# Kernel tuning notes

Measured on AMD Instinct MI355X. Metric: run time of the kernel, lower is better.

Reference implementation:

```python
import jax, jax.numpy as jnp
import numpy as np

N_POINTS = 1024
BETA = 0.75
N_IMP = int(BETA * N_POINTS)  # 768


def point_sample(feat, points):
    """Bilinear sample feat [B,C,H,W] at points [B,N,2] in [0,1] (x,y order).
    Matches F.grid_sample(feat, 2*points-1, align_corners=False, padding_mode='zeros')."""
    B, C, H, W = feat.shape
    gx = 2.0 * points[..., 0] - 1.0
    gy = 2.0 * points[..., 1] - 1.0
    # align_corners=False unnormalization
    x = ((gx + 1.0) * W - 1.0) * 0.5
    y = ((gy + 1.0) * H - 1.0) * 0.5
    x0 = jnp.floor(x)
    y0 = jnp.floor(y)
    wx = x - x0  # weight for x0+1
    wy = y - y0

    def gather(ix, iy):
        valid = (ix >= 0) & (ix <= W - 1) & (iy >= 0) & (iy <= H - 1)
        ixc = jnp.clip(ix, 0, W - 1).astype(jnp.int32)
        iyc = jnp.clip(iy, 0, H - 1).astype(jnp.int32)
        v = jax.vmap(lambda f, yy, xx: f[:, yy, xx])(feat, iyc, ixc)  # [B,C,N]
        return v * valid[:, None, :].astype(feat.dtype)

    v00 = gather(x0, y0)
    v01 = gather(x0 + 1, y0)
    v10 = gather(x0, y0 + 1)
    v11 = gather(x0 + 1, y0 + 1)
    wx_ = wx[:, None, :]
    wy_ = wy[:, None, :]
    return (v00 * (1 - wx_) * (1 - wy_) + v01 * wx_ * (1 - wy_)
            + v10 * (1 - wx_) * wy_ + v11 * wx_ * wy_)  # [B,C,N]


def sampling_points_train(coarse, over_gen, coverage):
    # sort channels descending per pixel, then sample the sorted map (PointRend)
    coarse_sorted = -jnp.sort(-coarse, axis=1)
    samp = point_sample(coarse_sorted, over_gen)  # [B,C,kN]
    uncertainty = -(samp[:, 0, :] - samp[:, 1, :])  # [B,kN]
    _, idx = jax.lax.top_k(uncertainty, N_IMP)  # [B,768]
    importance = jnp.take_along_axis(over_gen, idx[..., None], axis=1)  # [B,768,2]
    return jnp.concatenate([importance, coverage], axis=1)  # [B,1024,2]


def setup_inputs() -> dict:
    key = jax.random.key(0)
    ks = jax.random.split(key, 8)
    B = 16
    fine = jax.random.normal(ks[0], (B, 128, 256, 256), dtype=jnp.float32)
    coarse = jax.random.normal(ks[1], (B, 7, 64, 64), dtype=jnp.float32)
    w1 = jax.random.normal(ks[2], (135, 256), dtype=jnp.float32) * 0.05
    b1 = jnp.zeros((256,), dtype=jnp.float32)
    w2 = jax.random.normal(ks[3], (256, 7), dtype=jnp.float32) * 0.05
    b2 = jnp.zeros((7,), dtype=jnp.float32)
    over_gen = jax.random.uniform(ks[4], (B, 7 * N_POINTS, 2), dtype=jnp.float32)
    coverage = jax.random.uniform(ks[5], (B, N_POINTS - N_IMP, 2), dtype=jnp.float32)
    return {"fine": fine, "coarse": coarse, "w1": w1, "b1": b1,
            "w2": w2, "b2": b2, "over_gen": over_gen, "coverage": coverage}


def reference(fine, coarse, w1, b1, w2, b2, over_gen, coverage):
    points = sampling_points_train(coarse, over_gen, coverage)  # [B,1024,2]
    c = point_sample(coarse, points)  # [B,7,1024]
    f = point_sample(fine, points)    # [B,128,1024]
    feat = jnp.concatenate([c, f], axis=1).transpose(0, 2, 1)  # [B,1024,135]
    h = jax.nn.relu(jnp.einsum('bnc,cd->bnd', feat, w1) + b1)
    rend = (jnp.einsum('bnd,dk->bnk', h, w2) + b2).transpose(0, 2, 1)  # [B,7,1024]
    return rend, points
```

## Files before the change

kernel.cpp:

```cpp
#include <hip/hip_runtime.h>
#include <cstdint>
#include <cstddef>

#define PTS_OFF 114688

__global__ __launch_bounds__(1024) void select_points_kernel(
    const float* __restrict__ coarse,
    const float* __restrict__ over_gen,
    const float* __restrict__ coverage,
    float* out)
{
  const int b   = blockIdx.x;
  const int tid = threadIdx.x;

  __shared__ float sT1[4096];
  __shared__ float sT2[4096];
  __shared__ unsigned long long cand[1024];
  __shared__ unsigned int hist[1024];
  __shared__ int sSel;
  __shared__ int sRnew;
  __shared__ unsigned int sCnt;

  const float* cb = coarse + (size_t)b * 28672;
  for (int pix = tid; pix < 4096; pix += 1024) {
    float m1 = -INFINITY, m2 = -INFINITY;
#pragma unroll
    for (int ch = 0; ch < 7; ++ch) {
      float v = cb[ch * 4096 + pix];
      if (v > m1) { m2 = m1; m1 = v; }
      else if (v > m2) { m2 = v; }
    }
    sT1[pix] = m1;
    sT2[pix] = m2;
  }
  if (tid == 0) sCnt = 0u;
  __syncthreads();

  unsigned long long key[7];
  const float* og = over_gen + (size_t)b * 14336;
#pragma unroll
  for (int s = 0; s < 7; ++s) {
    int i = tid + s * 1024;
    float px = og[i * 2];
    float py = og[i * 2 + 1];
    float gx = __fsub_rn(__fmul_rn(2.0f, px), 1.0f);
    float gy = __fsub_rn(__fmul_rn(2.0f, py), 1.0f);
    float x  = __fmul_rn(__fsub_rn(__fmul_rn(__fadd_rn(gx, 1.0f), 64.0f), 1.0f), 0.5f);
    float y  = __fmul_rn(__fsub_rn(__fmul_rn(__fadd_rn(gy, 1.0f), 64.0f), 1.0f), 0.5f);
    float x0 = floorf(x), y0 = floorf(y);
    float wx = __fsub_rn(x, x0), wy = __fsub_rn(y, y0);
    float omwx = __fsub_rn(1.0f, wx), omwy = __fsub_rn(1.0f, wy);
    float x1 = x0 + 1.0f, y1 = y0 + 1.0f;

    float cxs[4] = {x0, x1, x0, x1};
    float cys[4] = {y0, y0, y1, y1};
    float t1[4], t2[4];
#pragma unroll
    for (int c = 0; c < 4; ++c) {
      bool valid = (cxs[c] >= 0.0f) && (cxs[c] <= 63.0f) &&
                   (cys[c] >= 0.0f) && (cys[c] <= 63.0f);
      int xi = (int)fminf(fmaxf(cxs[c], 0.0f), 63.0f);
      int yi = (int)fminf(fmaxf(cys[c], 0.0f), 63.0f);
      float m = valid ? 1.0f : 0.0f;
      int p = yi * 64 + xi;
      t1[c] = __fmul_rn(sT1[p], m);
      t2[c] = __fmul_rn(sT2[p], m);
    }
    float s0 = __fadd_rn(__fadd_rn(__fadd_rn(
        __fmul_rn(__fmul_rn(t1[0], omwx), omwy),
        __fmul_rn(__fmul_rn(t1[1], wx),   omwy)),
        __fmul_rn(__fmul_rn(t1[2], omwx), wy)),
        __fmul_rn(__fmul_rn(t1[3], wx),   wy));
    float s1 = __fadd_rn(__fadd_rn(__fadd_rn(
        __fmul_rn(__fmul_rn(t2[0], omwx), omwy),
        __fmul_rn(__fmul_rn(t2[1], wx),   omwy)),
        __fmul_rn(__fmul_rn(t2[2], omwx), wy)),
        __fmul_rn(__fmul_rn(t2[3], wx),   wy));
    float u = -__fsub_rn(s0, s1);
    unsigned int bits = __float_as_uint(u);
    unsigned int asc  = (bits & 0x80000000u) ? ~bits : (bits | 0x80000000u);
    unsigned int desc = ~asc;
    key[s] = ((unsigned long long)desc << 13) | (unsigned int)i;
  }

  unsigned int P = 0u;
  unsigned int r = 768u;
  const int sub = ((tid >> 6) & 3) << 8;
  for (int pos = 3; pos >= 0; --pos) {
    const int shift = pos * 8;
    hist[tid] = 0u;
    __syncthreads();
#pragma unroll
    for (int s = 0; s < 7; ++s) {
      unsigned int d = (unsigned int)(key[s] >> 13);
      if ((((d ^ P) >> shift) >> 8) == 0u) {
        atomicAdd(&hist[sub | ((d >> shift) & 255u)], 1u);
      }
    }
    __syncthreads();
    if (tid < 64) {
      unsigned int v0 = hist[tid*4]   + hist[256+tid*4]   + hist[512+tid*4]   + hist[768+tid*4];
      unsigned int v1 = hist[tid*4+1] + hist[256+tid*4+1] + hist[512+tid*4+1] + hist[768+tid*4+1];
      unsigned int v2 = hist[tid*4+2] + hist[256+tid*4+2] + hist[512+tid*4+2] + hist[768+tid*4+2];
      unsigned int v3 = hist[tid*4+3] + hist[256+tid*4+3] + hist[512+tid*4+3] + hist[768+tid*4+3];
      v1 += v0; v2 += v1; v3 += v2;
      unsigned int lanesum = v3;
      unsigned int inc = lanesum;
#pragma unroll
      for (int d = 1; d < 64; d <<= 1) {
        unsigned int tsum = __shfl_up(inc, d, 64);
        if (tid >= d) inc += tsum;
      }
      unsigned int excl = inc - lanesum;
      v0 += excl; v1 += excl; v2 += excl; v3 += excl;
      if (excl < r && r <= v0) { sSel = tid * 4;     sRnew = (int)(r - excl); }
      if (v0   < r && r <= v1) { sSel = tid * 4 + 1; sRnew = (int)(r - v0);   }
      if (v1   < r && r <= v2) { sSel = tid * 4 + 2; sRnew = (int)(r - v1);   }
      if (v2   < r && r <= v3) { sSel = tid * 4 + 3; sRnew = (int)(r - v2);   }
    }
    __syncthreads();
    P |= ((unsigned int)sSel) << shift;
    r = (unsigned int)sRnew;
  }

  cand[tid] = 0xFFFFFFFFFFFFFFFFull;
  __syncthreads();
#pragma unroll
  for (int s = 0; s < 7; ++s) {
    if ((unsigned int)(key[s] >> 13) <= P) {
      unsigned int p = atomicAdd(&sCnt, 1u);
      if (p < 1024u) cand[p] = key[s];
    }
  }
  __syncthreads();

  {
    unsigned long long e = cand[tid];
#pragma unroll
    for (int kk = 2; kk <= 64; kk <<= 1) {
      for (int j = kk >> 1; j >= 1; j >>= 1) {
        unsigned long long p = __shfl_xor(e, j, 64);
        bool up    = ((tid & kk) == 0);
        bool lower = ((tid & j) == 0);
        bool takemin = (lower == up);
        unsigned long long mn = (e < p) ? e : p;
        unsigned long long mx = (e < p) ? p : e;
        e = takemin ? mn : mx;
      }
    }
    cand[tid] = e;
    __syncthreads();

    for (int kk = 128; kk <= 1024; kk <<= 1) {
      for (int j = kk >> 1; j >= 64; j >>= 1) {
        int ixj = tid ^ j;
        if (ixj > tid) {
          unsigned long long a = cand[tid];
          unsigned long long c = cand[ixj];
          bool up = ((tid & kk) == 0);
          if ((a > c) == up) { cand[tid] = c; cand[ixj] = a; }
        }
        __syncthreads();
      }
      e = cand[tid];
      bool up = ((tid & kk) == 0);
#pragma unroll
      for (int j = 32; j >= 1; j >>= 1) {
        unsigned long long p = __shfl_xor(e, j, 64);
        bool lower = ((tid & j) == 0);
        bool takemin = (lower == up);
        unsigned long long mn = (e < p) ? e : p;
        unsigned long long mx = (e < p) ? p : e;
        e = takemin ? mn : mx;
      }
      cand[tid] = e;
      __syncthreads();
    }
  }

  float* po = out + PTS_OFF + (size_t)b * 2048;
  if (tid < 768) {
    unsigned int idx = (unsigned int)(cand[tid] & 0x1FFFu);
    po[tid * 2]     = og[idx * 2];
    po[tid * 2 + 1] = og[idx * 2 + 1];
  } else {
    int j = tid - 768;
    po[tid * 2]     = coverage[(size_t)b * 512 + j * 2];
    po[tid * 2 + 1] = coverage[(size_t)b * 512 + j * 2 + 1];
  }
}

__global__ __launch_bounds__(256) void point_head_kernel(
    const float* __restrict__ fine,
    const float* __restrict__ coarse,
    const float* __restrict__ gw1,
    const float* __restrict__ gb1,
    const float* __restrict__ gw2,
    const float* __restrict__ gb2,
    float* out)
{
  const int t   = threadIdx.x;
  const int blk = blockIdx.x;
  const int b   = blk >> 6;
  const int n0  = (blk & 63) * 16;

  __shared__ float sFeat[16][137];

  const float* pts = out + PTS_OFF + (size_t)b * 2048;
  const float* fb  = fine   + (size_t)b * 8388608;
  const float* cbs = coarse + (size_t)b * 28672;

  {
    const int pt = t & 15;
    const int cg = t >> 4;
    float px = pts[(n0 + pt) * 2];
    float py = pts[(n0 + pt) * 2 + 1];

    float gx = 2.0f * px - 1.0f;
    float gy = 2.0f * py - 1.0f;
    float x  = ((gx + 1.0f) * 256.0f - 1.0f) * 0.5f;
    float y  = ((gy + 1.0f) * 256.0f - 1.0f) * 0.5f;
    float x0f = floorf(x), y0f = floorf(y);
    float wx = x - x0f, wy = y - y0f;
    int ix0 = (int)x0f, iy0 = (int)y0f;
    int ix1 = ix0 + 1,  iy1 = iy0 + 1;
    float mx0 = (ix0 >= 0 && ix0 <= 255) ? 1.0f : 0.0f;
    float mx1 = (ix1 >= 0 && ix1 <= 255) ? 1.0f : 0.0f;
    float my0 = (iy0 >= 0 && iy0 <= 255) ? 1.0f : 0.0f;
    float my1 = (iy1 >= 0 && iy1 <= 255) ? 1.0f : 0.0f;
    int cx0 = min(max(ix0, 0), 255), cx1 = min(max(ix1, 0), 255);
    int cy0 = min(max(iy0, 0), 255), cy1 = min(max(iy1, 0), 255);
    float W00 = (1.0f - wx) * (1.0f - wy) * mx0 * my0;
    float W01 = wx * (1.0f - wy) * mx1 * my0;
    float W10 = (1.0f - wx) * wy * mx0 * my1;
    float W11 = wx * wy * mx1 * my1;
    int o00 = cy0 * 256 + cx0, o01 = cy0 * 256 + cx1;
    int o10 = cy1 * 256 + cx0, o11 = cy1 * 256 + cx1;

#pragma unroll
    for (int i = 0; i < 8; ++i) {
      int ch = cg * 8 + i;
      const float* f = fb + (size_t)ch * 65536;
      sFeat[pt][7 + ch] = f[o00] * W00 + f[o01] * W01 + f[o10] * W10 + f[o11] * W11;
    }

    if (cg == 0) {
      float cx  = ((gx + 1.0f) * 64.0f - 1.0f) * 0.5f;
      float cy  = ((gy + 1.0f) * 64.0f - 1.0f) * 0.5f;
      float cx0f = floorf(cx), cy0f = floorf(cy);
      float cwx = cx - cx0f, cwy = cy - cy0f;
      int jx0 = (int)cx0f, jy0 = (int)cy0f;
      int jx1 = jx0 + 1,   jy1 = jy0 + 1;
      float nx0 = (jx0 >= 0 && jx0 <= 63) ? 1.0f : 0.0f;
      float nx1 = (jx1 >= 0 && jx1 <= 63) ? 1.0f : 0.0f;
      float ny0 = (jy0 >= 0 && jy0 <= 63) ? 1.0f : 0.0f;
      float ny1 = (jy1 >= 0 && jy1 <= 63) ? 1.0f : 0.0f;
      int kx0 = min(max(jx0, 0), 63), kx1 = min(max(jx1, 0), 63);
      int ky0 = min(max(jy0, 0), 63), ky1 = min(max(jy1, 0), 63);
      float V00 = (1.0f - cwx) * (1.0f - cwy) * nx0 * ny0;
      float V01 = cwx * (1.0f - cwy) * nx1 * ny0;
      float V10 = (1.0f - cwx) * cwy * nx0 * ny1;
      float V11 = cwx * cwy * nx1 * ny1;
      int q00 = ky0 * 64 + kx0, q01 = ky0 * 64 + kx1;
      int q10 = ky1 * 64 + kx0, q11 = ky1 * 64 + kx1;
#pragma unroll
      for (int ch = 0; ch < 7; ++ch) {
        const float* c0 = cbs + ch * 4096;
        sFeat[pt][ch] = c0[q00] * V00 + c0[q01] * V01 + c0[q10] * V10 + c0[q11] * V11;
      }
    }
  }
  __syncthreads();

  const int lane = t & 63;
  const int wid  = t >> 6;
  const int p0   = wid * 4;

  float acc[4][4];
  {
    float bb0 = gb1[lane], bb1 = gb1[lane + 64];
    float bb2 = gb1[lane + 128], bb3 = gb1[lane + 192];
#pragma unroll
    for (int p = 0; p < 4; ++p) {
      acc[p][0] = bb0; acc[p][1] = bb1; acc[p][2] = bb2; acc[p][3] = bb3;
    }
  }
  for (int c = 0; c < 135; ++c) {
    const float* wr = gw1 + c * 256;
    float wv0 = wr[lane], wv1 = wr[lane + 64];
    float wv2 = wr[lane + 128], wv3 = wr[lane + 192];
#pragma unroll
    for (int p = 0; p < 4; ++p) {
      float fv = sFeat[p0 + p][c];
      acc[p][0] = fmaf(fv, wv0, acc[p][0]);
      acc[p][1] = fmaf(fv, wv1, acc[p][1]);
      acc[p][2] = fmaf(fv, wv2, acc[p][2]);
      acc[p][3] = fmaf(fv, wv3, acc[p][3]);
    }
  }

  float w2v[4][7];
#pragma unroll
  for (int rr = 0; rr < 4; ++rr) {
    const float* wr = gw2 + (size_t)(lane + 64 * rr) * 7;
#pragma unroll
    for (int k = 0; k < 7; ++k) w2v[rr][k] = wr[k];
  }
  float b2s = (lane < 7) ? gb2[lane] : 0.0f;

#pragma unroll
  for (int p = 0; p < 4; ++p) {
    float part[7];
#pragma unroll
    for (int k = 0; k < 7; ++k) part[k] = 0.0f;
#pragma unroll
    for (int rr = 0; rr < 4; ++rr) {
      float h = fmaxf(acc[p][rr], 0.0f);
#pragma unroll
      for (int k = 0; k < 7; ++k) part[k] = fmaf(h, w2v[rr][k], part[k]);
    }
#pragma unroll
    for (int k = 0; k < 7; ++k) {
      float s = part[k];
#pragma unroll
      for (int off = 32; off > 0; off >>= 1) s += __shfl_xor(s, off, 64);
      if (lane == k) out[((size_t)b * 7 + k) * 1024 + (n0 + p0 + p)] = s + b2s;
    }
  }
}

extern "C" void kernel_launch(void* const* d_in, const int* in_sizes, int n_in,
                              void* d_out, int out_size, void* d_ws, size_t ws_size,
                              hipStream_t stream) {
  (void)in_sizes; (void)n_in; (void)d_ws; (void)ws_size; (void)out_size;
  const float* fine     = (const float*)d_in[0];
  const float* coarse   = (const float*)d_in[1];
  const float* w1       = (const float*)d_in[2];
  const float* b1       = (const float*)d_in[3];
  const float* w2       = (const float*)d_in[4];
  const float* b2       = (const float*)d_in[5];
  const float* over_gen = (const float*)d_in[6];
  const float* coverage = (const float*)d_in[7];
  float* out = (float*)d_out;

  select_points_kernel<<<16, 1024, 0, stream>>>(coarse, over_gen, coverage, out);
  point_head_kernel<<<1024, 256, 0, stream>>>(fine, coarse, w1, b1, w2, b2, out);
}
```

Baseline: 710.1 us.

## Split point head into parallel gather kernel and larger-tile MLP kernel via workspace

Replaces the fused point_head kernel with two kernels. A gather kernel assigns 32 threads per point to bilinearly sample fine and coarse features into a workspace buffer, which exposes more memory-level parallelism for the scattered fine-map loads. An MLP kernel then processes 64 points per block, so each W1 load is reused across more points. The cost is an extra launch and a round trip of the 16384x136 feature matrix through global memory, and the new path only runs if the workspace is large enough.

```diff
diff --git a/kernel.cpp b/kernel.cpp
--- a/kernel.cpp
+++ b/kernel.cpp
@@ -3,6 +3,8 @@
 #include <cstddef>
 
 #define PTS_OFF 114688
+#define WS_ROW 136
+#define WS_NEEDED (16384u * WS_ROW * 4u)
 
 __global__ __launch_bounds__(1024) void select_points_kernel(
     const float* __restrict__ coarse,
@@ -162,18 +164,18 @@
         }
         __syncthreads();
       }
-      e = cand[tid];
+      unsigned long long e2 = cand[tid];
       bool up = ((tid & kk) == 0);
 #pragma unroll
       for (int j = 32; j >= 1; j >>= 1) {
-        unsigned long long p = __shfl_xor(e, j, 64);
+        unsigned long long p = __shfl_xor(e2, j, 64);
         bool lower = ((tid & j) == 0);
         bool takemin = (lower == up);
-        unsigned long long mn = (e < p) ? e : p;
-        unsigned long long mx = (e < p) ? p : e;
-        e = takemin ? mn : mx;
+        unsigned long long mn = (e2 < p) ? e2 : p;
+        unsigned long long mx = (e2 < p) ? p : e2;
+        e2 = takemin ? mn : mx;
       }
-      cand[tid] = e;
+      cand[tid] = e2;
       __syncthreads();
     }
   }
@@ -187,6 +189,162 @@
     int j = tid - 768;
     po[tid * 2]     = coverage[(size_t)b * 512 + j * 2];
     po[tid * 2 + 1] = coverage[(size_t)b * 512 + j * 2 + 1];
+  }
+}
+
+__global__ __launch_bounds__(256) void gather_feat_kernel(
+    const float* __restrict__ fine,
+    const float* __restrict__ coarse,
+    const float* __restrict__ outbuf,
+    float* __restrict__ ws)
+{
+  const int g   = blockIdx.x * 256 + threadIdx.x;
+  const int pt  = g >> 5;
+  const int sub = g & 31;
+  const int b   = pt >> 10;
+  const int n   = pt & 1023;
+
+  const float* pts = outbuf + PTS_OFF + (size_t)b * 2048;
+  const float* fb  = fine   + (size_t)b * 8388608;
+  const float* cbs = coarse + (size_t)b * 28672;
+  float* wrow = ws + (size_t)pt * WS_ROW;
+
+  float px = pts[n * 2];
+  float py = pts[n * 2 + 1];
+
+  float gx = 2.0f * px - 1.0f;
+  float gy = 2.0f * py - 1.0f;
+  float x  = ((gx + 1.0f) * 256.0f - 1.0f) * 0.5f;
+  float y  = ((gy + 1.0f) * 256.0f - 1.0f) * 0.5f;
+  float x0f = floorf(x), y0f = floorf(y);
+  float wx = x - x0f, wy = y - y0f;
+  int ix0 = (int)x0f, iy0 = (int)y0f;
+  int ix1 = ix0 + 1,  iy1 = iy0 + 1;
+  float mx0 = (ix0 >= 0 && ix0 <= 255) ? 1.0f : 0.0f;
+  float mx1 = (ix1 >= 0 && ix1 <= 255) ? 1.0f : 0.0f;
+  float my0 = (iy0 >= 0 && iy0 <= 255) ? 1.0f : 0.0f;
+  float my1 = (iy1 >= 0 && iy1 <= 255) ? 1.0f : 0.0f;
+  int cx0 = min(max(ix0, 0), 255), cx1 = min(max(ix1, 0), 255);
+  int cy0 = min(max(iy0, 0), 255), cy1 = min(max(iy1, 0), 255);
+  float W00 = (1.0f - wx) * (1.0f - wy) * mx0 * my0;
+  float W01 = wx * (1.0f - wy) * mx1 * my0;
+  float W10 = (1.0f - wx) * wy * mx0 * my1;
+  float W11 = wx * wy * mx1 * my1;
+  int o00 = cy0 * 256 + cx0, o01 = cy0 * 256 + cx1;
+  int o10 = cy1 * 256 + cx0, o11 = cy1 * 256 + cx1;
+
+#pragma unroll
+  for (int i = 0; i < 4; ++i) {
+    int ch = sub * 4 + i;
+    const float* f = fb + (size_t)ch * 65536;
+    wrow[7 + ch] = f[o00] * W00 + f[o01] * W01 + f[o10] * W10 + f[o11] * W11;
+  }
+
+  if (sub < 7) {
+    float cx  = ((gx + 1.0f) * 64.0f - 1.0f) * 0.5f;
+    float cy  = ((gy + 1.0f) * 64.0f - 1.0f) * 0.5f;
+    float cx0f = floorf(cx), cy0f = floorf(cy);
+    float cwx = cx - cx0f, cwy = cy - cy0f;
+    int jx0 = (int)cx0f, jy0 = (int)cy0f;
+    int jx1 = jx0 + 1,   jy1 = jy0 + 1;
+    float nx0 = (jx0 >= 0 && jx0 <= 63) ? 1.0f : 0.0f;
+    float nx1 = (jx1 >= 0 && jx1 <= 63) ? 1.0f : 0.0f;
+    float ny0 = (jy0 >= 0 && jy0 <= 63) ? 1.0f : 0.0f;
+    float ny1 = (jy1 >= 0 && jy1 <= 63) ? 1.0f : 0.0f;
+    int kx0 = min(max(jx0, 0), 63), kx1 = min(max(jx1, 0), 63);
+    int ky0 = min(max(jy0, 0), 63), ky1 = min(max(jy1, 0), 63);
+    float V00 = (1.0f - cwx) * (1.0f - cwy) * nx0 * ny0;
+    float V01 = cwx * (1.0f - cwy) * nx1 * ny0;
+    float V10 = (1.0f - cwx) * cwy * nx0 * ny1;
+    float V11 = cwx * cwy * nx1 * ny1;
+    int q00 = ky0 * 64 + kx0, q01 = ky0 * 64 + kx1;
+    int q10 = ky1 * 64 + kx0, q11 = ky1 * 64 + kx1;
+    const float* c0 = cbs + sub * 4096;
+    wrow[sub] = c0[q00] * V00 + c0[q01] * V01 + c0[q10] * V10 + c0[q11] * V11;
+  }
+}
+
+__global__ __launch_bounds__(256) void mlp_head_kernel(
+    const float* __restrict__ ws,
+    const float* __restrict__ gw1,
+    const float* __restrict__ gb1,
+    const float* __restrict__ gw2,
+    const float* __restrict__ gb2,
+    float* __restrict__ out)
+{
+  const int t   = threadIdx.x;
+  const int blk = blockIdx.x;
+  const int b   = blk >> 4;
+  const int n0  = (blk & 15) * 64;
+
+  __shared__ float sFeat[64][137];
+
+  const float4* src = (const float4*)(ws + (size_t)(b * 1024 + n0) * WS_ROW);
+  for (int v = t; v < 64 * 34; v += 256) {
+    int row = v / 34;
+    int col = v - row * 34;
+    float4 q = src[(size_t)row * 34 + col];
+    sFeat[row][col * 4 + 0] = q.x;
+    sFeat[row][col * 4 + 1] = q.y;
+    sFeat[row][col * 4 + 2] = q.z;
+    sFeat[row][col * 4 + 3] = q.w;
+  }
+  __syncthreads();
+
+  const int lane = t & 63;
+  const int wid  = t >> 6;
+  const int p0   = wid * 16;
+
+  float acc[16][4];
+  {
+    float bb0 = gb1[lane], bb1 = gb1[lane + 64];
+    float bb2 = gb1[lane + 128], bb3 = gb1[lane + 192];
+#pragma unroll
+    for (int p = 0; p < 16; ++p) {
+      acc[p][0] = bb0; acc[p][1] = bb1; acc[p][2] = bb2; acc[p][3] = bb3;
+    }
+  }
+  for (int c = 0; c < 135; ++c) {
+    const float* wr = gw1 + c * 256;
+    float wv0 = wr[lane], wv1 = wr[lane + 64];
+    float wv2 = wr[lane + 128], wv3 = wr[lane + 192];
+#pragma unroll
+    for (int p = 0; p < 16; ++p) {
+      float fv = sFeat[p0 + p][c];
+      acc[p][0] = fmaf(fv, wv0, acc[p][0]);
+      acc[p][1] = fmaf(fv, wv1, acc[p][1]);
+      acc[p][2] = fmaf(fv, wv2, acc[p][2]);
+      acc[p][3] = fmaf(fv, wv3, acc[p][3]);
+    }
+  }
+
+  float w2v[4][7];
+#pragma unroll
+  for (int rr = 0; rr < 4; ++rr) {
+    const float* wr = gw2 + (size_t)(lane + 64 * rr) * 7;
+#pragma unroll
+    for (int k = 0; k < 7; ++k) w2v[rr][k] = wr[k];
+  }
+  float b2s = (lane < 7) ? gb2[lane] : 0.0f;
+
+#pragma unroll
+  for (int p = 0; p < 16; ++p) {
+    float part[7];
+#pragma unroll
+    for (int k = 0; k < 7; ++k) part[k] = 0.0f;
+#pragma unroll
+    for (int rr = 0; rr < 4; ++rr) {
+      float h = fmaxf(acc[p][rr], 0.0f);
+#pragma unroll
+      for (int k = 0; k < 7; ++k) part[k] = fmaf(h, w2v[rr][k], part[k]);
+    }
+#pragma unroll
+    for (int k = 0; k < 7; ++k) {
+      float s = part[k];
+#pragma unroll
+      for (int off = 32; off > 0; off >>= 1) s += __shfl_xor(s, off, 64);
+      if (lane == k) out[((size_t)b * 7 + k) * 1024 + (n0 + p0 + p)] = s + b2s;
+    }
   }
 }
 
@@ -332,7 +490,7 @@
 extern "C" void kernel_launch(void* const* d_in, const int* in_sizes, int n_in,
                               void* d_out, int out_size, void* d_ws, size_t ws_size,
                               hipStream_t stream) {
-  (void)in_sizes; (void)n_in; (void)d_ws; (void)ws_size; (void)out_size;
+  (void)in_sizes; (void)n_in; (void)out_size;
   const float* fine     = (const float*)d_in[0];
   const float* coarse   = (const float*)d_in[1];
   const float* w1       = (const float*)d_in[2];
@@ -344,5 +502,12 @@
   float* out = (float*)d_out;
 
   select_points_kernel<<<16, 1024, 0, stream>>>(coarse, over_gen, coverage, out);
-  point_head_kernel<<<1024, 256, 0, stream>>>(fine, coarse, w1, b1, w2, b2, out);
+
+  if (d_ws != nullptr && ws_size >= (size_t)WS_NEEDED) {
+    float* ws = (float*)d_ws;
+    gather_feat_kernel<<<2048, 256, 0, stream>>>(fine, coarse, out, ws);
+    mlp_head_kernel<<<256, 256, 0, stream>>>(ws, w1, b1, w2, b2, out);
+  } else {
+    point_head_kernel<<<1024, 256, 0, stream>>>(fine, coarse, w1, b1, w2, b2, out);
+  }
 }
```

Measured after the change: 776.0 us. 1.09x slower.
